# Optimization experiments

Hardware: AMD Instinct MI355X
Metric: run time of the kernel (lower is better)

## Reference

```python
import jax, jax.numpy as jnp
import numpy as np

B_, G_, H_ = 16, 4096, 128
D_INNER, D_STATE, NHEADS, HEADDIM, CHUNK, D_CONV = 256, 16, 4, 64, 64, 4
LATENT = 64
D_IN_PROJ = 2 * D_INNER + 2 * D_STATE + NHEADS  # 548
CONV_DIM = D_INNER + 2 * D_STATE                # 288
NLAYERS = 4  # [fwd0, fwd1, bwd0, bwd1]
EPS = 1e-5


def _segsum(x):
    # x: (..., T) -> (..., T, T) stable segment sums, -inf above diagonal
    T = x.shape[-1]
    xe = jnp.broadcast_to(x[..., None], x.shape + (T,))
    lo = jnp.tril(jnp.ones((T, T), bool), -1)
    s = jnp.cumsum(jnp.where(lo, xe, 0.0), axis=-2)
    keep = jnp.tril(jnp.ones((T, T), bool), 0)
    return jnp.where(keep, s, -jnp.inf)


def _ssd(x, A, B, C):
    # x: (b, L, h, p), A: (b, L, h), B/C: (b, L, n)  (single shared head for B/C)
    b, L, h, p = x.shape
    c = L // CHUNK
    x = x.reshape(b, c, CHUNK, h, p)
    A = A.reshape(b, c, CHUNK, h).transpose(0, 3, 1, 2)  # b h c l
    B = B.reshape(b, c, CHUNK, -1)                       # b c l n
    C = C.reshape(b, c, CHUNK, -1)
    A_cs = jnp.cumsum(A, axis=-1)
    Lmat = jnp.exp(_segsum(A))                           # b h c l s
    Y_diag = jnp.einsum('bcln,bcsn,bhcls,bcshp->bclhp', C, B, Lmat, x)
    decay_states = jnp.exp(A_cs[:, :, :, -1:] - A_cs)
    states = jnp.einsum('bcln,bhcl,bclhp->bchpn', B, decay_states, x)
    states = jnp.concatenate([jnp.zeros_like(states[:, :1]), states], axis=1)
    decay_chunk = jnp.exp(_segsum(jnp.pad(A_cs[:, :, :, -1], ((0, 0), (0, 0), (1, 0)))))
    new_states = jnp.einsum('bhzc,bchpn->bzhpn', decay_chunk, states)
    states = new_states[:, :-1]
    sdo = jnp.exp(A_cs)
    Y_off = jnp.einsum('bcln,bchpn,bhcl->bclhp', C, states, sdo)
    return (Y_diag + Y_off).reshape(b, L, h, p)


def _mamba2(u, Wi, cw, cb, dtb, Alog, Dp, nw, Wo):
    b, L, _ = u.shape
    zxbcdt = u @ Wi.T                                   # (b, L, 548)
    z = zxbcdt[..., :D_INNER]
    xBC = zxbcdt[..., D_INNER:D_INNER + CONV_DIM]
    dt = jax.nn.softplus(zxbcdt[..., D_INNER + CONV_DIM:] + dtb)  # (b, L, h)
    # depthwise causal conv1d, padding=d_conv-1, keep first L outputs
    xt = xBC.transpose(0, 2, 1)
    y = jax.lax.conv_general_dilated(xt, cw[:, None, :], (1,), [(D_CONV - 1, D_CONV - 1)],
                                     dimension_numbers=('NCH', 'OIH', 'NCH'),
                                     feature_group_count=CONV_DIM)
    xBC = jax.nn.silu((y[:, :, :L] + cb[None, :, None]).transpose(0, 2, 1))
    x = xBC[..., :D_INNER].reshape(b, L, NHEADS, HEADDIM)
    Bm = xBC[..., D_INNER:D_INNER + D_STATE]
    Cm = xBC[..., D_INNER + D_STATE:]
    A = -jnp.exp(Alog)                                  # (h,)
    yssd = _ssd(x * dt[..., None], A * dt, Bm, Cm)
    yssd = yssd + x * Dp[:, None]
    yf = yssd.reshape(b, L, D_INNER)
    yf = yf * jax.nn.silu(z)                            # gated RMSNorm
    yf = yf * jax.lax.rsqrt(jnp.mean(yf * yf, -1, keepdims=True) + EPS) * nw
    return yf @ Wo.T


def _forward(expression, noise, expr_w, expr_b, in_proj_w, conv_w, conv_b, dt_bias,
             A_log, D_par, norm_w, out_proj_w, fusion_w, fusion_b, lm_w, lm_b,
             lv_w, lv_b, gate_w, gate_b, outp_w, outp_b, reg_gate):
    x = expression[..., None] * expr_w[:, 0] + expr_b   # Linear(1, H) -> (b, G, H)
    fwd = x
    for i in (0, 1):
        fwd = _mamba2(fwd, in_proj_w[i], conv_w[i], conv_b[i], dt_bias[i],
                      A_log[i], D_par[i], norm_w[i], out_proj_w[i])
    bwd = x[:, ::-1]
    for i in (2, 3):
        bwd = _mamba2(bwd, in_proj_w[i], conv_w[i], conv_b[i], dt_bias[i],
                      A_log[i], D_par[i], norm_w[i], out_proj_w[i])
    bwd = bwd[:, ::-1]
    fused = jax.nn.gelu(jnp.concatenate([fwd, bwd], -1) @ fusion_w.T + fusion_b,
                        approximate=False)
    lm = fused @ lm_w.T + lm_b
    lv = fused @ lv_w.T + lv_b
    sample = lm + noise * jnp.exp(0.5 * lv)             # reparameterize
    gate = jax.nn.sigmoid(sample @ gate_w.T + gate_b)
    h = fused * gate
    pred = (h @ outp_w.T + outp_b)[..., 0] * jax.nn.sigmoid(reg_gate)
    return pred, lm, lv, sample


def setup_inputs() -> dict:
    key = jax.random.key(0)
    ks = jax.random.split(key, 24)
    def w(k, shape, s=0.02):
        return jax.random.normal(k, shape, jnp.float32) * s
    return dict(
        expression=jax.random.uniform(ks[0], (B_, G_), jnp.float32),
        noise=jax.random.normal(ks[1], (B_, G_, LATENT), jnp.float32),
        expr_w=w(ks[2], (H_, 1), 0.2), expr_b=w(ks[3], (H_,)),
        in_proj_w=w(ks[4], (NLAYERS, D_IN_PROJ, H_)),
        conv_w=w(ks[5], (NLAYERS, CONV_DIM, D_CONV), 0.1),
        conv_b=w(ks[6], (NLAYERS, CONV_DIM)),
        dt_bias=jax.random.uniform(ks[7], (NLAYERS, NHEADS), jnp.float32, -4.0, 1.0),
        A_log=jnp.full((NLAYERS, NHEADS), -jnp.log(2.0), jnp.float32),
        D_par=jnp.ones((NLAYERS, NHEADS), jnp.float32),
        norm_w=jnp.ones((NLAYERS, D_INNER), jnp.float32),
        out_proj_w=w(ks[8], (NLAYERS, H_, D_INNER)),
        fusion_w=w(ks[9], (H_, 2 * H_)), fusion_b=w(ks[10], (H_,)),
        lm_w=w(ks[11], (LATENT, H_)), lm_b=w(ks[12], (LATENT,)),
        lv_w=w(ks[13], (LATENT, H_)), lv_b=w(ks[14], (LATENT,)),
        gate_w=w(ks[15], (H_, LATENT)), gate_b=w(ks[16], (H_,)),
        outp_w=w(ks[17], (1, H_)), outp_b=w(ks[18], (1,)),
        reg_gate=w(ks[19], (G_,), 0.01),
    )


def reference(expression, noise, expr_w, expr_b, in_proj_w, conv_w, conv_b, dt_bias,
              A_log, D_par, norm_w, out_proj_w, fusion_w, fusion_b, lm_w, lm_b,
              lv_w, lv_b, gate_w, gate_b, outp_w, outp_b, reg_gate):
    return _forward(expression, noise, expr_w, expr_b, in_proj_w, conv_w, conv_b,
                    dt_bias, A_log, D_par, norm_w, out_proj_w, fusion_w, fusion_b,
                    lm_w, lm_b, lv_w, lv_b, gate_w, gate_b, outp_w, outp_b, reg_gate)
```

## Files before the change

kernel.cpp:

```cpp
#include <hip/hip_runtime.h>
#include <math.h>

#define HMOD 128
#define DIN 256
#define NHEADS 4
#define HD 64
#define DSTATE 16
#define NCH 64
#define CONVD 288
#define DPROJ 548
#define LAT 64
#define LSEQ 4096

typedef __attribute__((ext_vector_type(8))) short bf16x8;
typedef __attribute__((ext_vector_type(4))) float f32x4;
typedef __attribute__((ext_vector_type(8))) unsigned short u16x8;
typedef __attribute__((ext_vector_type(4))) unsigned short u16x4;

__device__ __forceinline__ float sigm(float x){ return 1.0f/(1.0f+__expf(-x)); }
__device__ __forceinline__ float siluf(float x){ return x/(1.0f+__expf(-x)); }
__device__ __forceinline__ float softplusf(float x){ return (x>20.0f)? x : log1pf(expf(x)); }
__device__ __forceinline__ float geluf(float x){ return 0.5f*x*(1.0f+erff(x*0.70710678118654752440f)); }
__device__ __forceinline__ unsigned short f2bf(float x){
  unsigned int u = __float_as_uint(x);
  return (unsigned short)((u + 0x7FFFu + ((u>>16)&1u)) >> 16);
}
__device__ __forceinline__ float bf2f(unsigned short h){
  return __uint_as_float(((unsigned int)h)<<16);
}

__global__ __launch_bounds__(256) void cvt_kernel(const float* __restrict__ in,
  unsigned short* __restrict__ out, int n)
{
  int i = blockIdx.x*256 + threadIdx.x;
  if (i < n) out[i] = f2bf(in[i]);
}
__global__ __launch_bounds__(256) void cvt_nw_kernel(const float* __restrict__ in,
  const float* __restrict__ nw, unsigned short* __restrict__ out, int n)
{
  int i = blockIdx.x*256 + threadIdx.x;
  if (i < n){
    int k = i & 255;
    int li = i >> 15;
    out[i] = f2bf(in[i]*nw[li*256 + k]);
  }
}
__global__ __launch_bounds__(256) void cvt_cw_kernel(const float* __restrict__ in,
  float* __restrict__ out)
{
  int i = blockIdx.x*256 + threadIdx.x;
  if (i < 4608){
    int li = i/1152, r = i - li*1152;
    int ch = r>>2, k = r&3;
    out[li*1152 + k*CONVD + ch] = in[i];
  }
}

__global__ __launch_bounds__(256) void embed_kernel(const float* __restrict__ expr,
    const float* __restrict__ ew, const float* __restrict__ eb,
    unsigned short* __restrict__ actA, unsigned short* __restrict__ actB)
{
  int gid = blockIdx.x*256 + threadIdx.x;
  int m = gid >> 7, hh = gid & 127;
  int bl = m >> 12, g = m & 4095;
  unsigned short v = f2bf(expr[m]*ew[hh] + eb[hh]);
  actA[gid] = v;
  actB[(size_t)(((bl<<12) | (4095-g))<<7) + hh] = v;
}

template<int KDIM, int NT, int EPI>
__global__ __launch_bounds__(256) void gemm3(
    const unsigned short* __restrict__ A,
    const unsigned short* __restrict__ A2,
    const unsigned short* __restrict__ Wb,
    const float* __restrict__ bias,
    const float* __restrict__ bias2,
    const float* __restrict__ ssqp,
    unsigned short* __restrict__ ob1,
    unsigned short* __restrict__ ob2,
    float* __restrict__ of1,
    float* __restrict__ of2,
    const float* __restrict__ nzp,
    float* __restrict__ of3,
    int N, int ldc)
{
  __shared__ unsigned short Ws[64*(KDIM+8)];
  __shared__ __align__(16) unsigned short Cb[(EPI==5) ? 8 : 128*72];
  const int tid = threadIdx.x;
  const int m0 = blockIdx.x<<7;
  const int wid = tid>>6, lane = tid&63;
  const int la = lane&15, kq = lane>>4;
  const int mw = m0 + wid*32;

  bf16x8 af[KDIM/32][2];
  #pragma unroll
  for (int ki=0; ki<KDIM/32; ki++){
    int k = ki*32 + kq*8;
    #pragma unroll
    for (int mf=0; mf<2; mf++){
      int row = mw + mf*16 + la;
      const unsigned short* src;
      if (EPI==2){
        if (k < 128) src = A + (size_t)row*128 + k;
        else { int bl2=row>>12, t=row&4095; src = A2 + (size_t)(((bl2<<12)|(4095-t)))*128 + (k-128); }
      } else {
        src = A + (size_t)row*KDIM + k;
      }
      af[ki][mf] = *(const bf16x8*)src;
    }
  }
  float scv[2];
  if (EPI==4){
    #pragma unroll
    for (int mf=0; mf<2; mf++){
      int m = mw + mf*16 + la;
      float4 s4 = *(const float4*)&ssqp[m*4];
      scv[mf] = rsqrtf((s4.x+s4.y+s4.z+s4.w)*(1.0f/256.0f) + 1e-5f);
    }
  }
  f32x4 vlm[2][4];

  const int KD8 = KDIM/8;
  for (int nt=0; nt<NT; nt++){
    int n0 = (blockIdx.y*NT + nt)<<6;
    for (int ci = tid; ci < 64*KD8; ci += 256){
      int row = ci/KD8, kc = (ci - row*KD8)*8;
      int n = n0 + row;
      bf16x8 v = {0,0,0,0,0,0,0,0};
      if (n < N) v = *(const bf16x8*)&Wb[(size_t)n*KDIM + kc];
      *(bf16x8*)&Ws[row*(KDIM+8) + kc] = v;
    }
    __syncthreads();
    f32x4 acc[2][4] = {};
    #pragma unroll
    for (int ki=0; ki<KDIM/32; ki++){
      #pragma unroll
      for (int nf=0; nf<4; nf++){
        bf16x8 wfr = *(const bf16x8*)&Ws[(nf*16 + la)*(KDIM+8) + ki*32 + kq*8];
        #pragma unroll
        for (int mf=0; mf<2; mf++)
          acc[mf][nf] = __builtin_amdgcn_mfma_f32_16x16x32_bf16(wfr, af[ki][mf], acc[mf][nf], 0,0,0);
      }
    }
    #pragma unroll
    for (int mf=0; mf<2; mf++){
      #pragma unroll
      for (int nf=0; nf<4; nf++){
        int m   = mw + mf*16 + la;
        int row = wid*32 + mf*16 + la;
        int colb = nf*16 + kq*4;
        int nb  = n0 + colb;
        f32x4 v = acc[mf][nf];
        if (EPI==1){
          if (nb >= DIN+CONVD){
            if (nb < DPROJ){
              float4 o;
              o.x = softplusf(v[0] + bias[0]); o.y = softplusf(v[1] + bias[1]);
              o.z = softplusf(v[2] + bias[2]); o.w = softplusf(v[3] + bias[3]);
              *(float4*)&of1[(size_t)m*NHEADS] = o;
            }
          } else {
            u16x4 p; p[0]=f2bf(v[0]); p[1]=f2bf(v[1]); p[2]=f2bf(v[2]); p[3]=f2bf(v[3]);
            *(u16x4*)&Cb[row*72 + colb] = p;
          }
        } else if (EPI==2){
          float4 b4 = *(const float4*)&bias[nb];
          u16x4 p;
          p[0]=f2bf(geluf(v[0]+b4.x)); p[1]=f2bf(geluf(v[1]+b4.y));
          p[2]=f2bf(geluf(v[2]+b4.z)); p[3]=f2bf(geluf(v[3]+b4.w));
          *(u16x4*)&Cb[row*72 + colb] = p;
        } else if (EPI==4){
          u16x4 p;
          p[0]=f2bf(v[0]*scv[mf]); p[1]=f2bf(v[1]*scv[mf]);
          p[2]=f2bf(v[2]*scv[mf]); p[3]=f2bf(v[3]*scv[mf]);
          *(u16x4*)&Cb[row*72 + colb] = p;
        } else if (EPI==5){
          if (nt == 0){
            float4 b4 = *(const float4*)&bias[colb];
            f32x4 lm; lm[0]=v[0]+b4.x; lm[1]=v[1]+b4.y; lm[2]=v[2]+b4.z; lm[3]=v[3]+b4.w;
            vlm[mf][nf] = lm;
            *(f32x4*)&of1[(size_t)m*64 + colb] = lm;
          } else {
            float4 b4 = *(const float4*)&bias2[colb];
            f32x4 lv; lv[0]=v[0]+b4.x; lv[1]=v[1]+b4.y; lv[2]=v[2]+b4.z; lv[3]=v[3]+b4.w;
            *(f32x4*)&of2[(size_t)m*64 + colb] = lv;
            f32x4 nz = *(const f32x4*)&nzp[(size_t)m*64 + colb];
            f32x4 sp;
            #pragma unroll
            for (int j=0;j<4;j++) sp[j] = fmaf(nz[j], expf(0.5f*lv[j]), vlm[mf][nf][j]);
            *(f32x4*)&of3[(size_t)m*64 + colb] = sp;
          }
        }
      }
    }
    if (EPI!=5){
      __syncthreads();
      #pragma unroll
      for (int j=0; j<4; j++){
        int row = (tid>>3) + j*32;
        int col0 = (tid&7)*8;
        int m = m0 + row;
        int nch = n0 + col0;
        u16x8 val = *(const u16x8*)&Cb[row*72 + col0];
        if (EPI==1){
          if (nch < DIN)            *(u16x8*)&ob1[(size_t)m*DIN + nch] = val;
          else if (nch < DIN+CONVD) *(u16x8*)&ob2[(size_t)m*CONVD + (nch-DIN)] = val;
        } else {
          *(u16x8*)&ob1[(size_t)m*ldc + nch] = val;
        }
      }
    }
    __syncthreads();
  }
}

__global__ __launch_bounds__(256) void conv_kernel(const unsigned short* __restrict__ xraw,
  const float* __restrict__ cwT, const float* __restrict__ cb,
  unsigned short* __restrict__ xconv)
{
  int gid = blockIdx.x*256 + threadIdx.x;
  int m = gid / 36, v = gid - (gid/36)*36;
  int ch0 = v*8;
  int t = m & 4095;
  float acc[8];
  float4 b0 = *(const float4*)&cb[ch0];
  float4 b1 = *(const float4*)&cb[ch0+4];
  acc[0]=b0.x; acc[1]=b0.y; acc[2]=b0.z; acc[3]=b0.w;
  acc[4]=b1.x; acc[5]=b1.y; acc[6]=b1.z; acc[7]=b1.w;
  #pragma unroll
  for (int k=0;k<4;k++){
    int tt = t - 3 + k;
    if (tt >= 0){
      u16x8 xv = *(const u16x8*)&xraw[(size_t)(m-3+k)*CONVD + ch0];
      float4 w0 = *(const float4*)&cwT[k*CONVD + ch0];
      float4 w1 = *(const float4*)&cwT[k*CONVD + ch0 + 4];
      float w[8] = {w0.x,w0.y,w0.z,w0.w,w1.x,w1.y,w1.z,w1.w};
      #pragma unroll
      for (int j=0;j<8;j++) acc[j] = fmaf(w[j], bf2f(xv[j]), acc[j]);
    }
  }
  u16x8 o;
  #pragma unroll
  for (int j=0;j<8;j++) o[j] = f2bf(siluf(acc[j]));
  *(u16x8*)&xconv[(size_t)m*CONVD + ch0] = o;
}

__global__ __launch_bounds__(256) void ssd_front(
  const unsigned short* __restrict__ xconv, const float* __restrict__ dtsp,
  const float* __restrict__ Alog,
  float* __restrict__ states_g, float* __restrict__ acs_g, float* __restrict__ atot_g)
{
  __shared__ __align__(16) unsigned short Xt[64*88];
  __shared__ __align__(16) unsigned short Raw[64*72];
  __shared__ __align__(16) unsigned short Braw[64*24];
  __shared__ __align__(16) unsigned short Bwt[16*88];
  __shared__ float acs_s[64], dts_s[64];
  const int bx = blockIdx.x;
  const int h = bx & 3, c = (bx>>2)&63, bl = bx>>8;
  const int tid = threadIdx.x;
  const int tokbase = (bl<<12) + (c<<6);

  if (tid < 64) {
    float dt = dtsp[(size_t)(tokbase+tid)*NHEADS + h];
    dts_s[tid] = dt;
    float xsc = -__expf(Alog[h]) * dt;
    #pragma unroll
    for (int off=1; off<64; off<<=1){ float v = __shfl_up(xsc, off); if (tid >= off) xsc += v; }
    acs_s[tid] = xsc;
    acs_g[(size_t)bx*64 + tid] = xsc;
  }
  #pragma unroll
  for (int i=0;i<2;i++){
    int idx = tid + (i<<8);
    int l = idx>>3, g = idx&7;
    *(u16x8*)&Raw[l*72 + g*8] = *(const u16x8*)&xconv[(size_t)(tokbase+l)*CONVD + h*64 + g*8];
  }
  if (tid < 128){
    int l = tid>>1, half = tid&1;
    *(u16x8*)&Braw[l*24 + half*8] = *(const u16x8*)&xconv[(size_t)(tokbase+l)*CONVD + 256 + half*8];
  }
  __syncthreads();
  const float atotv = acs_s[63];
  if (tid==0) atot_g[bx] = atotv;
  #pragma unroll
  for (int i=0;i<2;i++){
    int u = tid + (i<<8);
    int ch = u & 63, l0 = (u>>6)*8;
    u16x8 o;
    #pragma unroll
    for (int j=0;j<8;j++) o[j] = Raw[(l0+j)*72 + ch];
    *(u16x8*)&Xt[ch*88 + l0] = o;
  }
  if (tid < 128){
    int ch = tid & 15, l0 = (tid>>4)*8;
    u16x8 o;
    #pragma unroll
    for (int j=0;j<8;j++){
      int l = l0+j;
      o[j] = f2bf(bf2f(Braw[l*24 + ch]) * __expf(atotv - acs_s[l]) * dts_s[l]);
    }
    *(u16x8*)&Bwt[ch*88 + l0] = o;
  }
  __syncthreads();
  const int wid = tid>>6, lane = tid&63;
  const int la = lane&15, kq = lane>>4;
  f32x4 acc = {0.f,0.f,0.f,0.f};
  #pragma unroll
  for (int kt=0; kt<2; kt++){
    bf16x8 a = *(const bf16x8*)&Xt[(wid*16+la)*88 + kt*32+kq*8];
    bf16x8 b = *(const bf16x8*)&Bwt[la*88 + kt*32+kq*8];
    acc = __builtin_amdgcn_mfma_f32_16x16x32_bf16(a, b, acc, 0,0,0);
  }
  size_t base = (size_t)bx<<10;
  #pragma unroll
  for (int r=0;r<4;r++){
    int p = wid*16 + kq*4 + r;
    states_g[base + (size_t)p*16 + la] = acc[r];
  }
}

__global__ __launch_bounds__(256) void scan_kernel(float* __restrict__ states,
  const float* __restrict__ atot)
{
  int gid = blockIdx.x*256 + threadIdx.x;
  int inner = gid & 1023;
  int h = (gid>>10)&3;
  int bl = gid>>12;
  size_t base = (size_t)bl*262144 + h*1024 + inner;
  int abase = bl*256 + h;
  float v[64];
  #pragma unroll
  for (int c2=0;c2<64;c2++) v[c2] = states[base + (size_t)c2*4096];
  float S = 0.0f;
  #pragma unroll
  for (int c2=0;c2<64;c2++){
    states[base + (size_t)c2*4096] = S;
    S = __expf(atot[abase + c2*4])*S + v[c2];
  }
}

__global__ __launch_bounds__(256) void ssd_back(
  const unsigned short* __restrict__ xconv, const unsigned short* __restrict__ zb,
  const float* __restrict__ dtsp, const float* __restrict__ acs_g,
  const float* __restrict__ states, const float* __restrict__ Dp,
  unsigned short* __restrict__ yf, float* __restrict__ ssqp)
{
  __shared__ __align__(16) unsigned short U[2*64*72];
  __shared__ __align__(16) unsigned short CBS[3*64*40];
  __shared__ float acs_s[64], dts_s[64];
  unsigned short* Xt = U;
  unsigned short* Sb = U + 64*72;
  unsigned short* Cp = CBS;
  unsigned short* Bp = CBS + 64*40;
  unsigned short* Sp = CBS + 2*64*40;
  float* Yl = (float*)U;
  const int bx = blockIdx.x;
  const int h = bx & 3, c = (bx>>2)&63, bl = bx>>8;
  const int tid = threadIdx.x;
  const int tokbase = (bl<<12) + (c<<6);

  if (tid < 64) {
    dts_s[tid] = dtsp[(size_t)(tokbase+tid)*NHEADS + h];
    acs_s[tid] = acs_g[(size_t)bx*64 + tid];
  }
  for (int i = tid; i < 1024; i += 256){
    int l = i>>4, k = 16 + (i&15);
    Cp[l*40+k] = 0; Bp[l*40+k] = 0; Sp[l*40+k] = 0;
  }
  #pragma unroll
  for (int i=0;i<2;i++){
    int idx = tid + (i<<8);
    int l = idx>>3, g = idx&7;
    *(u16x8*)&Sb[l*72 + g*8] = *(const u16x8*)&xconv[(size_t)(tokbase+l)*CONVD + h*64 + g*8];
  }
  {
    int l = tid>>2, part = tid&3;
    u16x8 vv = *(const u16x8*)&xconv[(size_t)(tokbase+l)*CONVD + 256 + part*8];
    if (part < 2) *(u16x8*)&Bp[l*40 + part*8] = vv;
    else          *(u16x8*)&Cp[l*40 + (part-2)*8] = vv;
  }
  #pragma unroll
  for (int i=0;i<4;i++){
    int e = tid + (i<<8);
    int p = e>>4, n = e&15;
    Sp[p*40+n] = f2bf(states[((size_t)bx<<10) + e]);
  }
  __syncthreads();
  #pragma unroll
  for (int i=0;i<2;i++){
    int u = tid + (i<<8);
    int ch = u & 63, l0 = (u>>6)*8;
    u16x8 o;
    #pragma unroll
    for (int j=0;j<8;j++) o[j] = Sb[(l0+j)*72 + ch];
    *(u16x8*)&Xt[ch*72 + l0] = o;
  }
  __syncthreads();

  const int wid = tid>>6, lane = tid&63;
  const int la = lane&15, kq = lane>>4;
  const int L0 = wid*16;
  const f32x4 zero4 = {0.f,0.f,0.f,0.f};
  const float Dh = Dp[h];

  {
    bf16x8 a = *(const bf16x8*)&Cp[(L0+la)*40 + kq*8];
    f32x4 cbacc[4];
    #pragma unroll
    for (int nf=0; nf<4; nf++){
      bf16x8 b = *(const bf16x8*)&Bp[(nf*16+la)*40 + kq*8];
      cbacc[nf] = __builtin_amdgcn_mfma_f32_16x16x32_bf16(a, b, zero4, 0,0,0);
    }
    #pragma unroll
    for (int nf=0; nf<4; nf++){
      #pragma unroll
      for (int r=0; r<4; r++){
        int l = L0 + kq*4 + r, s = nf*16 + la;
        float v = 0.f;
        if (s <= l) v = __expf(acs_s[l]-acs_s[s])*dts_s[s]*cbacc[nf][r];
        if (s == l) v += Dh;
        Sb[l*72 + s] = f2bf(v);
      }
    }
  }
  f32x4 ya[4];
  {
    bf16x8 a = *(const bf16x8*)&Cp[(L0+la)*40 + kq*8];
    #pragma unroll
    for (int nf=0; nf<4; nf++){
      bf16x8 b = *(const bf16x8*)&Sp[(nf*16+la)*40 + kq*8];
      ya[nf] = __builtin_amdgcn_mfma_f32_16x16x32_bf16(a, b, zero4, 0,0,0);
    }
    float eal[4];
    #pragma unroll
    for (int r=0; r<4; r++) eal[r] = __expf(acs_s[L0 + kq*4 + r]);
    #pragma unroll
    for (int nf=0; nf<4; nf++)
      #pragma unroll
      for (int r=0; r<4; r++) ya[nf][r] *= eal[r];
  }
  #pragma unroll
  for (int kt=0; kt<2; kt++){
    bf16x8 a = *(const bf16x8*)&Sb[(L0+la)*72 + kt*32+kq*8];
    #pragma unroll
    for (int nf=0; nf<4; nf++){
      bf16x8 b = *(const bf16x8*)&Xt[(nf*16+la)*72 + kt*32+kq*8];
      ya[nf] = __builtin_amdgcn_mfma_f32_16x16x32_bf16(a, b, ya[nf], 0,0,0);
    }
  }
  __syncthreads();
  #pragma unroll
  for (int nf=0; nf<4; nf++){
    #pragma unroll
    for (int r=0; r<4; r++){
      int l = L0 + kq*4 + r, p = nf*16 + la;
      Yl[l*68 + p] = ya[nf][r];
    }
  }
  __syncthreads();
  #pragma unroll
  for (int i=0;i<2;i++){
    int u = tid + (i<<8);
    int l = u>>3, g = u&7;
    size_t gidx = (size_t)(tokbase+l)*DIN + (h<<6) + g*8;
    u16x8 z8 = *(const u16x8*)&zb[gidx];
    u16x8 o8;
    float ps = 0.f;
    #pragma unroll
    for (int j=0;j<8;j++){
      float y = Yl[l*68 + g*8 + j];
      float zv = bf2f(z8[j]);
      float yv = y * zv * sigm(zv);
      o8[j] = f2bf(yv);
      ps = fmaf(yv, yv, ps);
    }
    *(u16x8*)&yf[gidx] = o8;
    ps += __shfl_xor(ps, 1); ps += __shfl_xor(ps, 2); ps += __shfl_xor(ps, 4);
    if (g == 0) ssqp[(size_t)(tokbase+l)*NHEADS + h] = ps;
  }
}

__global__ __launch_bounds__(256) void predgate_kernel(
  const unsigned short* __restrict__ fused, const float* __restrict__ sample,
  const unsigned short* __restrict__ gwb, const float* __restrict__ gb,
  const float* __restrict__ ow, const float* __restrict__ ob,
  const float* __restrict__ rg, float* __restrict__ pred)
{
  __shared__ __align__(16) unsigned short Ws[64*72];
  __shared__ __align__(16) float Gp[128*68];
  const int tid = threadIdx.x;
  const int m0 = blockIdx.x<<7;
  const int wid = tid>>6, lane = tid&63;
  const int la = lane&15, kq = lane>>4;
  const int mw = m0 + wid*32;

  bf16x8 af[2][2];
  #pragma unroll
  for (int ki=0; ki<2; ki++){
    int k = ki*32 + kq*8;
    #pragma unroll
    for (int mf=0; mf<2; mf++){
      int row = mw + mf*16 + la;
      float4 s0 = *(const float4*)&sample[(size_t)row*64 + k];
      float4 s1 = *(const float4*)&sample[(size_t)row*64 + k + 4];
      bf16x8 o;
      o[0]=(short)f2bf(s0.x); o[1]=(short)f2bf(s0.y); o[2]=(short)f2bf(s0.z); o[3]=(short)f2bf(s0.w);
      o[4]=(short)f2bf(s1.x); o[5]=(short)f2bf(s1.y); o[6]=(short)f2bf(s1.z); o[7]=(short)f2bf(s1.w);
      af[ki][mf] = o;
    }
  }
  const float ob0 = ob[0];
  const int prow = tid>>1, phalf = tid&1;
  float rs = 0.f;

  #pragma unroll
  for (int nt=0; nt<2; nt++){
    int n0 = nt<<6;
    #pragma unroll
    for (int i=0;i<2;i++){
      int slot = tid + (i<<8);
      int row = slot>>3, g = slot&7;
      *(u16x8*)&Ws[row*72 + g*8] = *(const u16x8*)&gwb[(size_t)(n0+row)*64 + g*8];
    }
    __syncthreads();
    f32x4 acc[2][4] = {};
    #pragma unroll
    for (int ki=0; ki<2; ki++){
      #pragma unroll
      for (int nf=0; nf<4; nf++){
        bf16x8 bfr = *(const bf16x8*)&Ws[(nf*16 + la)*72 + ki*32 + kq*8];
        #pragma unroll
        for (int mf=0; mf<2; mf++)
          acc[mf][nf] = __builtin_amdgcn_mfma_f32_16x16x32_bf16(af[ki][mf], bfr, acc[mf][nf], 0,0,0);
      }
    }
    #pragma unroll
    for (int mf=0; mf<2; mf++){
      #pragma unroll
      for (int nf=0; nf<4; nf++){
        #pragma unroll
        for (int r=0; r<4; r++){
          int row = wid*32 + mf*16 + kq*4 + r;
          int col = nf*16 + la;
          int n = n0 + col;
          Gp[row*68 + col] = sigm(acc[mf][nf][r] + gb[n]) * ow[n];
        }
      }
    }
    __syncthreads();
    #pragma unroll
    for (int q=0; q<4; q++){
      int col0 = phalf*32 + q*8;
      u16x8 f8 = *(const u16x8*)&fused[(size_t)(m0+prow)*128 + n0 + col0];
      float4 g0 = *(const float4*)&Gp[prow*68 + col0];
      float4 g1 = *(const float4*)&Gp[prow*68 + col0 + 4];
      rs = fmaf(bf2f(f8[0]), g0.x, rs); rs = fmaf(bf2f(f8[1]), g0.y, rs);
      rs = fmaf(bf2f(f8[2]), g0.z, rs); rs = fmaf(bf2f(f8[3]), g0.w, rs);
      rs = fmaf(bf2f(f8[4]), g1.x, rs); rs = fmaf(bf2f(f8[5]), g1.y, rs);
      rs = fmaf(bf2f(f8[6]), g1.z, rs); rs = fmaf(bf2f(f8[7]), g1.w, rs);
    }
    __syncthreads();
  }
  rs += __shfl_xor(rs, 1);
  if (phalf == 0){
    int m = m0 + prow;
    pred[m] = (rs + ob0) * sigm(rg[m & 4095]);
  }
}

extern "C" void kernel_launch(void* const* d_in, const int* in_sizes, int n_in,
                              void* d_out, int out_size, void* d_ws, size_t ws_size,
                              hipStream_t stream)
{
  const float* expr      = (const float*)d_in[0];
  const float* noise     = (const float*)d_in[1];
  const float* expr_w    = (const float*)d_in[2];
  const float* expr_b    = (const float*)d_in[3];
  const float* in_proj_w = (const float*)d_in[4];
  const float* conv_w    = (const float*)d_in[5];
  const float* conv_b    = (const float*)d_in[6];
  const float* dt_bias   = (const float*)d_in[7];
  const float* A_log     = (const float*)d_in[8];
  const float* D_par     = (const float*)d_in[9];
  const float* norm_w    = (const float*)d_in[10];
  const float* out_proj_w= (const float*)d_in[11];
  const float* fusion_w  = (const float*)d_in[12];
  const float* fusion_b  = (const float*)d_in[13];
  const float* lm_w      = (const float*)d_in[14];
  const float* lm_b      = (const float*)d_in[15];
  const float* lv_w      = (const float*)d_in[16];
  const float* lv_b      = (const float*)d_in[17];
  const float* gate_w    = (const float*)d_in[18];
  const float* gate_b    = (const float*)d_in[19];
  const float* outp_w    = (const float*)d_in[20];
  const float* outp_b    = (const float*)d_in[21];
  const float* reg_gate  = (const float*)d_in[22];

  const size_t WBYTES = 956416;
  int BG = 0;
  const int cands[5] = {16, 8, 4, 2, 1};
  for (int ci = 0; ci < 5; ci++) {
    int c2 = cands[ci];
    size_t MGc = (size_t)c2 * LSEQ;
    size_t need = WBYTES + MGc*2992 + (size_t)c2*1024 + 256;
    if (need <= ws_size) { BG = c2; break; }
  }
  if (!BG) return;
  const size_t MG = (size_t)BG * LSEQ;

  unsigned short* wip = (unsigned short*)d_ws;
  unsigned short* wop = wip + 280576;
  unsigned short* wfu = wop + 131072;
  unsigned short* wlm = wfu + 32768;
  unsigned short* wlv = wlm + 8192;
  unsigned short* wgw = wlv + 8192;
  float* cwT   = (float*)(wgw + 8192);
  float* dtsp  = (float*)((char*)d_ws + WBYTES);
  float* acs   = dtsp + MG*4;
  float* atot  = acs  + MG*4;
  float* states= atot + (size_t)BG*256;
  float* ssqp  = states + MG*64;
  unsigned short* zb    = (unsigned short*)(ssqp + MG*4);
  unsigned short* xrawb = zb    + MG*256;
  unsigned short* xcv   = xrawb + MG*288;
  unsigned short* actA  = xcv   + MG*288;
  unsigned short* actB  = actA  + MG*128;
  unsigned short* yfb   = actB  + MG*128;
  unsigned short* fusedbf = yfb;

  float* out_pred_g = (float*)d_out;
  float* out_lm_g   = out_pred_g + (size_t)16*LSEQ;
  float* out_lv_g   = out_lm_g   + (size_t)16*LSEQ*LAT;
  float* out_samp_g = out_lv_g   + (size_t)16*LSEQ*LAT;

  cvt_kernel<<<(280576+255)/256, 256, 0, stream>>>(in_proj_w, wip, 280576);
  cvt_nw_kernel<<<131072/256,    256, 0, stream>>>(out_proj_w, norm_w, wop, 131072);
  cvt_kernel<<<32768/256,        256, 0, stream>>>(fusion_w, wfu, 32768);
  cvt_kernel<<<8192/256,         256, 0, stream>>>(lm_w, wlm, 8192);
  cvt_kernel<<<8192/256,         256, 0, stream>>>(lv_w, wlv, 8192);
  cvt_kernel<<<8192/256,         256, 0, stream>>>(gate_w, wgw, 8192);
  cvt_cw_kernel<<<(4608+255)/256, 256, 0, stream>>>(conv_w, cwT);

  for (int b0 = 0; b0 < 16; b0 += BG) {
    float* out_pred = out_pred_g + (size_t)b0*LSEQ;
    float* out_lm   = out_lm_g   + (size_t)b0*LSEQ*LAT;
    float* out_lv   = out_lv_g   + (size_t)b0*LSEQ*LAT;
    float* out_samp = out_samp_g + (size_t)b0*LSEQ*LAT;
    const float* nz = noise      + (size_t)b0*LSEQ*LAT;

    embed_kernel<<<(MG*128)/256, 256, 0, stream>>>(expr + (size_t)b0*LSEQ, expr_w, expr_b, actA, actB);

    for (int li = 0; li < 4; li++) {
      unsigned short* u = (li < 2) ? actA : actB;
      const unsigned short* Wi = wip + (size_t)li*DPROJ*HMOD;
      const unsigned short* Wo = wop + (size_t)li*HMOD*DIN;
      const float* cwTl = cwT + (size_t)li*1152;
      const float* cb   = conv_b + (size_t)li*CONVD;
      const float* dtb  = dt_bias + (size_t)li*NHEADS;
      const float* Al   = A_log + (size_t)li*NHEADS;
      const float* Dl   = D_par + (size_t)li*NHEADS;

      gemm3<128,3,1><<<dim3(MG/128, 3), 256, 0, stream>>>(u, nullptr, Wi, dtb, nullptr, nullptr, zb, xrawb, dtsp, nullptr, nullptr, nullptr, DPROJ, 0);
      conv_kernel<<<(MG*36)/256, 256, 0, stream>>>(xrawb, cwTl, cb, xcv);
      ssd_front<<<BG*256, 256, 0, stream>>>(xcv, dtsp, Al, states, acs, atot);
      scan_kernel<<<(BG*LSEQ)/256, 256, 0, stream>>>(states, atot);
      ssd_back<<<BG*256, 256, 0, stream>>>(xcv, zb, dtsp, acs, states, Dl, yfb, ssqp);
      gemm3<256,1,4><<<dim3(MG/128, 2), 256, 0, stream>>>(yfb, nullptr, Wo, nullptr, nullptr, ssqp, u, nullptr, nullptr, nullptr, nullptr, nullptr, HMOD, HMOD);
    }

    gemm3<256,1,2><<<dim3(MG/128, 2), 256, 0, stream>>>(actA, actB, wfu, fusion_b, nullptr, nullptr, fusedbf, nullptr, nullptr, nullptr, nullptr, nullptr, HMOD, HMOD);
    gemm3<128,2,5><<<dim3(MG/128, 1), 256, 0, stream>>>(fusedbf, nullptr, wlm, lm_b, lv_b, nullptr, nullptr, nullptr, out_lm, out_lv, nz, out_samp, 128, LAT);
    predgate_kernel<<<MG/128, 256, 0, stream>>>(fusedbf, out_samp, wgw, gate_b, outp_w, outp_b, reg_gate, out_pred);
  }
}
```

Before: 612.8 us.

## Load GEMM weight fragments directly from global and use per-wave epilogue staging

The gemm3 kernel no longer stages the weight tile in shared memory. Each wave now loads its bf16 weight fragments straight from global memory, and each wave owns its own slice of the output staging buffer. That lets the block-wide barriers be replaced with a wave-local LDS wait, cutting LDS traffic, shared memory footprint and synchronisation. The cost is that every wave re-reads the same weights from global/L2 instead of sharing one LDS copy. A barrier is also added in the SSD kernel before the Sb/Xt MFMA loop, likely for correctness.

```diff
diff --git a/kernel.cpp b/kernel.cpp
--- a/kernel.cpp
+++ b/kernel.cpp
@@ -84,13 +84,13 @@
     float* __restrict__ of3,
     int N, int ldc)
 {
-  __shared__ unsigned short Ws[64*(KDIM+8)];
   __shared__ __align__(16) unsigned short Cb[(EPI==5) ? 8 : 128*72];
   const int tid = threadIdx.x;
   const int m0 = blockIdx.x<<7;
   const int wid = tid>>6, lane = tid&63;
   const int la = lane&15, kq = lane>>4;
   const int mw = m0 + wid*32;
+  unsigned short* Cw = (EPI==5) ? Cb : &Cb[wid*32*72];
 
   bf16x8 af[KDIM/32][2];
   #pragma unroll
@@ -120,23 +120,16 @@
   }
   f32x4 vlm[2][4];
 
-  const int KD8 = KDIM/8;
   for (int nt=0; nt<NT; nt++){
     int n0 = (blockIdx.y*NT + nt)<<6;
-    for (int ci = tid; ci < 64*KD8; ci += 256){
-      int row = ci/KD8, kc = (ci - row*KD8)*8;
-      int n = n0 + row;
-      bf16x8 v = {0,0,0,0,0,0,0,0};
-      if (n < N) v = *(const bf16x8*)&Wb[(size_t)n*KDIM + kc];
-      *(bf16x8*)&Ws[row*(KDIM+8) + kc] = v;
-    }
-    __syncthreads();
     f32x4 acc[2][4] = {};
     #pragma unroll
     for (int ki=0; ki<KDIM/32; ki++){
       #pragma unroll
       for (int nf=0; nf<4; nf++){
-        bf16x8 wfr = *(const bf16x8*)&Ws[(nf*16 + la)*(KDIM+8) + ki*32 + kq*8];
+        int n = n0 + nf*16 + la;
+        bf16x8 wfr = {0,0,0,0,0,0,0,0};
+        if (n < N) wfr = *(const bf16x8*)&Wb[(size_t)n*KDIM + ki*32 + kq*8];
         #pragma unroll
         for (int mf=0; mf<2; mf++)
           acc[mf][nf] = __builtin_amdgcn_mfma_f32_16x16x32_bf16(wfr, af[ki][mf], acc[mf][nf], 0,0,0);
@@ -146,10 +139,10 @@
     for (int mf=0; mf<2; mf++){
       #pragma unroll
       for (int nf=0; nf<4; nf++){
-        int m   = mw + mf*16 + la;
-        int row = wid*32 + mf*16 + la;
+        int m    = mw + mf*16 + la;
+        int rloc = mf*16 + la;
         int colb = nf*16 + kq*4;
-        int nb  = n0 + colb;
+        int nb   = n0 + colb;
         f32x4 v = acc[mf][nf];
         if (EPI==1){
           if (nb >= DIN+CONVD){
@@ -161,19 +154,19 @@
             }
           } else {
             u16x4 p; p[0]=f2bf(v[0]); p[1]=f2bf(v[1]); p[2]=f2bf(v[2]); p[3]=f2bf(v[3]);
-            *(u16x4*)&Cb[row*72 + colb] = p;
+            *(u16x4*)&Cw[rloc*72 + colb] = p;
           }
         } else if (EPI==2){
           float4 b4 = *(const float4*)&bias[nb];
           u16x4 p;
           p[0]=f2bf(geluf(v[0]+b4.x)); p[1]=f2bf(geluf(v[1]+b4.y));
           p[2]=f2bf(geluf(v[2]+b4.z)); p[3]=f2bf(geluf(v[3]+b4.w));
-          *(u16x4*)&Cb[row*72 + colb] = p;
+          *(u16x4*)&Cw[rloc*72 + colb] = p;
         } else if (EPI==4){
           u16x4 p;
           p[0]=f2bf(v[0]*scv[mf]); p[1]=f2bf(v[1]*scv[mf]);
           p[2]=f2bf(v[2]*scv[mf]); p[3]=f2bf(v[3]*scv[mf]);
-          *(u16x4*)&Cb[row*72 + colb] = p;
+          *(u16x4*)&Cw[rloc*72 + colb] = p;
         } else if (EPI==5){
           if (nt == 0){
             float4 b4 = *(const float4*)&bias[colb];
@@ -194,14 +187,14 @@
       }
     }
     if (EPI!=5){
-      __syncthreads();
+      asm volatile("s_waitcnt lgkmcnt(0)" ::: "memory");
       #pragma unroll
       for (int j=0; j<4; j++){
-        int row = (tid>>3) + j*32;
-        int col0 = (tid&7)*8;
-        int m = m0 + row;
+        int rloc = (lane>>3) + j*8;
+        int col0 = (lane&7)*8;
+        int m = mw + rloc;
         int nch = n0 + col0;
-        u16x8 val = *(const u16x8*)&Cb[row*72 + col0];
+        u16x8 val = *(const u16x8*)&Cw[rloc*72 + col0];
         if (EPI==1){
           if (nch < DIN)            *(u16x8*)&ob1[(size_t)m*DIN + nch] = val;
           else if (nch < DIN+CONVD) *(u16x8*)&ob2[(size_t)m*CONVD + (nch-DIN)] = val;
@@ -209,8 +202,8 @@
           *(u16x8*)&ob1[(size_t)m*ldc + nch] = val;
         }
       }
-    }
-    __syncthreads();
+      asm volatile("" ::: "memory");
+    }
   }
 }
 
@@ -439,6 +432,7 @@
       #pragma unroll
       for (int r=0; r<4; r++) ya[nf][r] *= eal[r];
   }
+  __syncthreads();
   #pragma unroll
   for (int kt=0; kt<2; kt++){
     bf16x8 a = *(const bf16x8*)&Sb[(L0+la)*72 + kt*32+kq*8];
```

New measurement: 748.0 us. +22.1%, slower.

## Batch fwd/bwd Mamba layers together, fuse conv into SSD kernels, bf16 states

Applied to the files above, without the earlier changes.

Each launch now runs the forward and backward stacks together over a doubled row range, with per-half weight and bias offsets, which halves the number of layer launches and enlarges the grids. The standalone depthwise conv kernel is removed and the conv plus SiLU is recomputed inside ssd_front and ssd_back straight from the raw projection. That drops the xconv buffer round trip but does the conv work twice. Inter-chunk states are kept in bf16 instead of fp32 to cut scan traffic, at some precision cost, and z and the gated output now share one buffer.

```diff
diff --git a/kernel.cpp b/kernel.cpp
--- a/kernel.cpp
+++ b/kernel.cpp
@@ -82,12 +82,13 @@
     float* __restrict__ of2,
     const float* __restrict__ nzp,
     float* __restrict__ of3,
-    int N, int ldc)
+    int N, int ldc, int mhalf, int wsel, int bsel)
 {
   __shared__ unsigned short Ws[64*(KDIM+8)];
   __shared__ __align__(16) unsigned short Cb[(EPI==5) ? 8 : 128*72];
   const int tid = threadIdx.x;
   const int m0 = blockIdx.x<<7;
+  if (m0 >= mhalf){ Wb += wsel; bias += bsel; }
   const int wid = tid>>6, lane = tid&63;
   const int la = lane&15, kq = lane>>4;
   const int mw = m0 + wid*32;
@@ -146,10 +147,10 @@
     for (int mf=0; mf<2; mf++){
       #pragma unroll
       for (int nf=0; nf<4; nf++){
-        int m   = mw + mf*16 + la;
-        int row = wid*32 + mf*16 + la;
+        int m    = mw + mf*16 + la;
+        int row  = wid*32 + mf*16 + la;
         int colb = nf*16 + kq*4;
-        int nb  = n0 + colb;
+        int nb   = n0 + colb;
         f32x4 v = acc[mf][nf];
         if (EPI==1){
           if (nb >= DIN+CONVD){
@@ -214,14 +215,10 @@
   }
 }
 
-__global__ __launch_bounds__(256) void conv_kernel(const unsigned short* __restrict__ xraw,
+__device__ __forceinline__ void conv8(const unsigned short* __restrict__ xraw,
   const float* __restrict__ cwT, const float* __restrict__ cb,
-  unsigned short* __restrict__ xconv)
-{
-  int gid = blockIdx.x*256 + threadIdx.x;
-  int m = gid / 36, v = gid - (gid/36)*36;
-  int ch0 = v*8;
-  int t = m & 4095;
+  int seqbase, int t, int ch0, u16x8* out)
+{
   float acc[8];
   float4 b0 = *(const float4*)&cb[ch0];
   float4 b1 = *(const float4*)&cb[ch0+4];
@@ -231,7 +228,7 @@
   for (int k=0;k<4;k++){
     int tt = t - 3 + k;
     if (tt >= 0){
-      u16x8 xv = *(const u16x8*)&xraw[(size_t)(m-3+k)*CONVD + ch0];
+      u16x8 xv = *(const u16x8*)&xraw[(size_t)(seqbase+tt)*CONVD + ch0];
       float4 w0 = *(const float4*)&cwT[k*CONVD + ch0];
       float4 w1 = *(const float4*)&cwT[k*CONVD + ch0 + 4];
       float w[8] = {w0.x,w0.y,w0.z,w0.w,w1.x,w1.y,w1.z,w1.w};
@@ -242,13 +239,15 @@
   u16x8 o;
   #pragma unroll
   for (int j=0;j<8;j++) o[j] = f2bf(siluf(acc[j]));
-  *(u16x8*)&xconv[(size_t)m*CONVD + ch0] = o;
+  *out = o;
 }
 
 __global__ __launch_bounds__(256) void ssd_front(
-  const unsigned short* __restrict__ xconv, const float* __restrict__ dtsp,
+  const unsigned short* __restrict__ xraw, const float* __restrict__ dtsp,
   const float* __restrict__ Alog,
-  float* __restrict__ states_g, float* __restrict__ acs_g, float* __restrict__ atot_g)
+  const float* __restrict__ cwT, const float* __restrict__ cb,
+  unsigned short* __restrict__ states_g, float* __restrict__ acs_g,
+  float* __restrict__ atot_g, int BGs)
 {
   __shared__ __align__(16) unsigned short Xt[64*88];
   __shared__ __align__(16) unsigned short Raw[64*72];
@@ -259,25 +258,31 @@
   const int h = bx & 3, c = (bx>>2)&63, bl = bx>>8;
   const int tid = threadIdx.x;
   const int tokbase = (bl<<12) + (c<<6);
+  const int seqbase = bl<<12;
+  const int s1 = (bl >= BGs);
+  const float* cwTs = cwT + (s1 ? 2304 : 0);
+  const float* cbs  = cb  + (s1 ? 576  : 0);
 
   if (tid < 64) {
     float dt = dtsp[(size_t)(tokbase+tid)*NHEADS + h];
     dts_s[tid] = dt;
-    float xsc = -__expf(Alog[h]) * dt;
+    float xsc = -__expf(Alog[(s1?8:0) + h]) * dt;
     #pragma unroll
     for (int off=1; off<64; off<<=1){ float v = __shfl_up(xsc, off); if (tid >= off) xsc += v; }
     acs_s[tid] = xsc;
     acs_g[(size_t)bx*64 + tid] = xsc;
   }
   #pragma unroll
-  for (int i=0;i<2;i++){
-    int idx = tid + (i<<8);
-    int l = idx>>3, g = idx&7;
-    *(u16x8*)&Raw[l*72 + g*8] = *(const u16x8*)&xconv[(size_t)(tokbase+l)*CONVD + h*64 + g*8];
-  }
-  if (tid < 128){
-    int l = tid>>1, half = tid&1;
-    *(u16x8*)&Braw[l*24 + half*8] = *(const u16x8*)&xconv[(size_t)(tokbase+l)*CONVD + 256 + half*8];
+  for (int i=0;i<3;i++){
+    int slot = tid + (i<<8);
+    if (slot < 640){
+      int l = slot/10, g = slot - (slot/10)*10;
+      int ch0 = (g<8) ? (h<<6)+g*8 : 256+(g-8)*8;
+      u16x8 o;
+      conv8(xraw, cwTs, cbs, seqbase, (c<<6)+l, ch0, &o);
+      if (g<8) *(u16x8*)&Raw[l*72 + g*8] = o;
+      else     *(u16x8*)&Braw[l*24 + (g-8)*8] = o;
+    }
   }
   __syncthreads();
   const float atotv = acs_s[63];
@@ -315,11 +320,11 @@
   #pragma unroll
   for (int r=0;r<4;r++){
     int p = wid*16 + kq*4 + r;
-    states_g[base + (size_t)p*16 + la] = acc[r];
-  }
-}
-
-__global__ __launch_bounds__(256) void scan_kernel(float* __restrict__ states,
+    states_g[base + (size_t)p*16 + la] = f2bf(acc[r]);
+  }
+}
+
+__global__ __launch_bounds__(256) void scan_kernel(unsigned short* __restrict__ states,
   const float* __restrict__ atot)
 {
   int gid = blockIdx.x*256 + threadIdx.x;
@@ -330,20 +335,21 @@
   int abase = bl*256 + h;
   float v[64];
   #pragma unroll
-  for (int c2=0;c2<64;c2++) v[c2] = states[base + (size_t)c2*4096];
+  for (int c2=0;c2<64;c2++) v[c2] = bf2f(states[base + (size_t)c2*4096]);
   float S = 0.0f;
   #pragma unroll
   for (int c2=0;c2<64;c2++){
-    states[base + (size_t)c2*4096] = S;
+    states[base + (size_t)c2*4096] = f2bf(S);
     S = __expf(atot[abase + c2*4])*S + v[c2];
   }
 }
 
 __global__ __launch_bounds__(256) void ssd_back(
-  const unsigned short* __restrict__ xconv, const unsigned short* __restrict__ zb,
+  const unsigned short* __restrict__ xraw, unsigned short* __restrict__ zyf,
   const float* __restrict__ dtsp, const float* __restrict__ acs_g,
-  const float* __restrict__ states, const float* __restrict__ Dp,
-  unsigned short* __restrict__ yf, float* __restrict__ ssqp)
+  const unsigned short* __restrict__ states, const float* __restrict__ Dp,
+  const float* __restrict__ cwT, const float* __restrict__ cb,
+  float* __restrict__ ssqp, int BGs)
 {
   __shared__ __align__(16) unsigned short U[2*64*72];
   __shared__ __align__(16) unsigned short CBS[3*64*40];
@@ -358,6 +364,11 @@
   const int h = bx & 3, c = (bx>>2)&63, bl = bx>>8;
   const int tid = threadIdx.x;
   const int tokbase = (bl<<12) + (c<<6);
+  const int seqbase = bl<<12;
+  const int s1 = (bl >= BGs);
+  const float* cwTs = cwT + (s1 ? 2304 : 0);
+  const float* cbs  = cb  + (s1 ? 576  : 0);
+  const float Dh = Dp[(s1?8:0) + h];
 
   if (tid < 64) {
     dts_s[tid] = dtsp[(size_t)(tokbase+tid)*NHEADS + h];
@@ -368,22 +379,21 @@
     Cp[l*40+k] = 0; Bp[l*40+k] = 0; Sp[l*40+k] = 0;
   }
   #pragma unroll
-  for (int i=0;i<2;i++){
-    int idx = tid + (i<<8);
-    int l = idx>>3, g = idx&7;
-    *(u16x8*)&Sb[l*72 + g*8] = *(const u16x8*)&xconv[(size_t)(tokbase+l)*CONVD + h*64 + g*8];
-  }
-  {
-    int l = tid>>2, part = tid&3;
-    u16x8 vv = *(const u16x8*)&xconv[(size_t)(tokbase+l)*CONVD + 256 + part*8];
-    if (part < 2) *(u16x8*)&Bp[l*40 + part*8] = vv;
-    else          *(u16x8*)&Cp[l*40 + (part-2)*8] = vv;
+  for (int i=0;i<3;i++){
+    int slot = tid + (i<<8);
+    int l = slot/12, g = slot - (slot/12)*12;
+    int ch0 = (g<8) ? (h<<6)+g*8 : 256+(g-8)*8;
+    u16x8 o;
+    conv8(xraw, cwTs, cbs, seqbase, (c<<6)+l, ch0, &o);
+    if (g<8)        *(u16x8*)&Sb[l*72 + g*8] = o;
+    else if (g<10)  *(u16x8*)&Bp[l*40 + (g-8)*8] = o;
+    else            *(u16x8*)&Cp[l*40 + (g-10)*8] = o;
   }
   #pragma unroll
   for (int i=0;i<4;i++){
     int e = tid + (i<<8);
     int p = e>>4, n = e&15;
-    Sp[p*40+n] = f2bf(states[((size_t)bx<<10) + e]);
+    Sp[p*40+n] = states[((size_t)bx<<10) + e];
   }
   __syncthreads();
   #pragma unroll
@@ -401,7 +411,6 @@
   const int la = lane&15, kq = lane>>4;
   const int L0 = wid*16;
   const f32x4 zero4 = {0.f,0.f,0.f,0.f};
-  const float Dh = Dp[h];
 
   {
     bf16x8 a = *(const bf16x8*)&Cp[(L0+la)*40 + kq*8];
@@ -463,7 +472,7 @@
     int u = tid + (i<<8);
     int l = u>>3, g = u&7;
     size_t gidx = (size_t)(tokbase+l)*DIN + (h<<6) + g*8;
-    u16x8 z8 = *(const u16x8*)&zb[gidx];
+    u16x8 z8 = *(const u16x8*)&zyf[gidx];
     u16x8 o8;
     float ps = 0.f;
     #pragma unroll
@@ -474,7 +483,7 @@
       o8[j] = f2bf(yv);
       ps = fmaf(yv, yv, ps);
     }
-    *(u16x8*)&yf[gidx] = o8;
+    *(u16x8*)&zyf[gidx] = o8;
     ps += __shfl_xor(ps, 1); ps += __shfl_xor(ps, 2); ps += __shfl_xor(ps, 4);
     if (g == 0) ssqp[(size_t)(tokbase+l)*NHEADS + h] = ps;
   }
@@ -597,16 +606,18 @@
   const float* reg_gate  = (const float*)d_in[22];
 
   const size_t WBYTES = 956416;
+  const int IMAX = 0x7fffffff;
   int BG = 0;
   const int cands[5] = {16, 8, 4, 2, 1};
   for (int ci = 0; ci < 5; ci++) {
     int c2 = cands[ci];
-    size_t MGc = (size_t)c2 * LSEQ;
-    size_t need = WBYTES + MGc*2992 + (size_t)c2*1024 + 256;
+    size_t MG2c = (size_t)2 * c2 * LSEQ;
+    size_t need = WBYTES + MG2c*1520 + (size_t)c2*2048 + 256;
     if (need <= ws_size) { BG = c2; break; }
   }
   if (!BG) return;
-  const size_t MG = (size_t)BG * LSEQ;
+  const size_t MG  = (size_t)BG * LSEQ;
+  const size_t MG2 = 2*MG;
 
   unsigned short* wip = (unsigned short*)d_ws;
   unsigned short* wop = wip + 280576;
@@ -616,17 +627,16 @@
   unsigned short* wgw = wlv + 8192;
   float* cwT   = (float*)(wgw + 8192);
   float* dtsp  = (float*)((char*)d_ws + WBYTES);
-  float* acs   = dtsp + MG*4;
-  float* atot  = acs  + MG*4;
-  float* states= atot + (size_t)BG*256;
-  float* ssqp  = states + MG*64;
-  unsigned short* zb    = (unsigned short*)(ssqp + MG*4);
-  unsigned short* xrawb = zb    + MG*256;
-  unsigned short* xcv   = xrawb + MG*288;
-  unsigned short* actA  = xcv   + MG*288;
-  unsigned short* actB  = actA  + MG*128;
-  unsigned short* yfb   = actB  + MG*128;
-  unsigned short* fusedbf = yfb;
+  float* acs   = dtsp + MG2*4;
+  float* atot  = acs  + MG2*4;
+  float* ssqp  = atot + (size_t)2*BG*256;
+  unsigned short* statesb = (unsigned short*)(ssqp + MG2*4);
+  unsigned short* zyf   = statesb + MG2*64;
+  unsigned short* xrawb = zyf + MG2*256;
+  unsigned short* act   = xrawb + MG2*288;
+  unsigned short* actA  = act;
+  unsigned short* actB  = act + MG*128;
+  unsigned short* fusedbf = zyf;
 
   float* out_pred_g = (float*)d_out;
   float* out_lm_g   = out_pred_g + (size_t)16*LSEQ;
@@ -650,26 +660,28 @@
 
     embed_kernel<<<(MG*128)/256, 256, 0, stream>>>(expr + (size_t)b0*LSEQ, expr_w, expr_b, actA, actB);
 
-    for (int li = 0; li < 4; li++) {
-      unsigned short* u = (li < 2) ? actA : actB;
-      const unsigned short* Wi = wip + (size_t)li*DPROJ*HMOD;
-      const unsigned short* Wo = wop + (size_t)li*HMOD*DIN;
-      const float* cwTl = cwT + (size_t)li*1152;
-      const float* cb   = conv_b + (size_t)li*CONVD;
-      const float* dtb  = dt_bias + (size_t)li*NHEADS;
-      const float* Al   = A_log + (size_t)li*NHEADS;
-      const float* Dl   = D_par + (size_t)li*NHEADS;
-
-      gemm3<128,3,1><<<dim3(MG/128, 3), 256, 0, stream>>>(u, nullptr, Wi, dtb, nullptr, nullptr, zb, xrawb, dtsp, nullptr, nullptr, nullptr, DPROJ, 0);
-      conv_kernel<<<(MG*36)/256, 256, 0, stream>>>(xrawb, cwTl, cb, xcv);
-      ssd_front<<<BG*256, 256, 0, stream>>>(xcv, dtsp, Al, states, acs, atot);
-      scan_kernel<<<(BG*LSEQ)/256, 256, 0, stream>>>(states, atot);
-      ssd_back<<<BG*256, 256, 0, stream>>>(xcv, zb, dtsp, acs, states, Dl, yfb, ssqp);
-      gemm3<256,1,4><<<dim3(MG/128, 2), 256, 0, stream>>>(yfb, nullptr, Wo, nullptr, nullptr, ssqp, u, nullptr, nullptr, nullptr, nullptr, nullptr, HMOD, HMOD);
-    }
-
-    gemm3<256,1,2><<<dim3(MG/128, 2), 256, 0, stream>>>(actA, actB, wfu, fusion_b, nullptr, nullptr, fusedbf, nullptr, nullptr, nullptr, nullptr, nullptr, HMOD, HMOD);
-    gemm3<128,2,5><<<dim3(MG/128, 1), 256, 0, stream>>>(fusedbf, nullptr, wlm, lm_b, lv_b, nullptr, nullptr, nullptr, out_lm, out_lv, nz, out_samp, 128, LAT);
+    for (int p = 0; p < 2; p++) {
+      const unsigned short* Wi = wip + (size_t)p*DPROJ*HMOD;
+      const unsigned short* Wo = wop + (size_t)p*HMOD*DIN;
+      const float* cwTl = cwT + (size_t)p*1152;
+      const float* cb   = conv_b + (size_t)p*CONVD;
+      const float* dtb  = dt_bias + (size_t)p*NHEADS;
+      const float* Al   = A_log + (size_t)p*NHEADS;
+      const float* Dl   = D_par + (size_t)p*NHEADS;
+
+      gemm3<128,3,1><<<dim3(MG2/128, 3), 256, 0, stream>>>(act, nullptr, Wi, dtb, nullptr, nullptr,
+        zyf, xrawb, dtsp, nullptr, nullptr, nullptr, DPROJ, 0, (int)MG, 2*DPROJ*HMOD, 2*NHEADS);
+      ssd_front<<<2*BG*256, 256, 0, stream>>>(xrawb, dtsp, Al, cwTl, cb, statesb, acs, atot, BG);
+      scan_kernel<<<(2*BG*LSEQ)/256, 256, 0, stream>>>(statesb, atot);
+      ssd_back<<<2*BG*256, 256, 0, stream>>>(xrawb, zyf, dtsp, acs, statesb, Dl, cwTl, cb, ssqp, BG);
+      gemm3<256,1,4><<<dim3(MG2/128, 2), 256, 0, stream>>>(zyf, nullptr, Wo, nullptr, nullptr, ssqp,
+        act, nullptr, nullptr, nullptr, nullptr, nullptr, HMOD, HMOD, (int)MG, 2*HMOD*DIN, 0);
+    }
+
+    gemm3<256,1,2><<<dim3(MG/128, 2), 256, 0, stream>>>(actA, actB, wfu, fusion_b, nullptr, nullptr,
+      fusedbf, nullptr, nullptr, nullptr, nullptr, nullptr, HMOD, HMOD, IMAX, 0, 0);
+    gemm3<128,2,5><<<dim3(MG/128, 1), 256, 0, stream>>>(fusedbf, nullptr, wlm, lm_b, lv_b, nullptr,
+      nullptr, nullptr, out_lm, out_lv, nz, out_samp, 128, LAT, IMAX, 0, 0);
     predgate_kernel<<<MG/128, 256, 0, stream>>>(fusedbf, out_samp, wgw, gate_b, outp_w, outp_b, reg_gate, out_pred);
   }
 }
```

Measured after the change: 598.9 us. 1.02x faster.
